# Kernel tuning notes

Hardware: AMD Instinct MI355X
Metric: run time of the kernel (lower is better)

Reference implementation:

```python
import jax, jax.numpy as jnp
import numpy as np

N_NODES = 50000
N_EDGES = 800000
IN_FEATS = 256
OUT_FEATS = 32
NUM_HEADS = 8
NUM_ETYPES = 5


def setup_inputs() -> dict:
    key = jax.random.key(0)
    k1, k2, k3, k4, k5, k6 = jax.random.split(key, 6)
    feat = jax.random.normal(k1, (N_NODES, IN_FEATS), dtype=jnp.float32)
    # xavier_normal-ish scale for fc weight [H*D, in]
    fc_w = jax.random.normal(k2, (NUM_HEADS * OUT_FEATS, IN_FEATS), dtype=jnp.float32) * 0.088
    edge_emb = jax.random.normal(k3, (NUM_ETYPES, NUM_HEADS), dtype=jnp.float32)
    e_feat = jax.random.randint(k4, (N_EDGES,), 0, NUM_ETYPES)
    src = jax.random.randint(k5, (N_EDGES,), 0, N_NODES)
    dst = jax.random.randint(k6, (N_EDGES,), 0, N_NODES)
    return {"feat": feat, "fc_w": fc_w, "edge_emb": edge_emb,
            "e_feat": e_feat, "src": src, "dst": dst}


def reference(feat, fc_w, edge_emb, e_feat, src, dst):
    N = feat.shape[0]
    H, D = NUM_HEADS, OUT_FEATS
    # fc: [N, in] @ [in, H*D] -> [N, H, D]
    feat_src = (feat @ fc_w.T).reshape(N, H, D)
    # per-edge, per-head logits from edge-type embedding: [E, H]
    e = edge_emb[e_feat]
    # edge_softmax: softmax over incoming edges of each dst node, per head
    m = jax.ops.segment_max(e, dst, num_segments=N)          # [N, H]
    ex = jnp.exp(e - m[dst])                                  # [E, H]
    denom = jax.ops.segment_sum(ex, dst, num_segments=N)     # [N, H]
    attn = ex / denom[dst]                                    # [E, H]
    # attn_sum: sum of attention weights arriving at each dst (== 1 w/o dropout)
    attn_sum = jax.ops.segment_sum(attn, dst, num_segments=N)  # [N, H]
    # weighted aggregation: sum_e attn_e * feat_src[src_e]
    msg = feat_src[src] * attn[:, :, None]                    # [E, H, D]
    agg = jax.ops.segment_sum(msg, dst, num_segments=N)      # [N, H, D]
    rst = agg / (attn_sum[:, :, None] + 1e-12)
    return rst, attn
```

## Files before the change

kernel.cpp:

```cpp
#include <hip/hip_runtime.h>

typedef unsigned short u16;
typedef unsigned int u32;
typedef __attribute__((ext_vector_type(8))) short bf16x8;
typedef __attribute__((ext_vector_type(4))) float f32x4;
typedef __attribute__((ext_vector_type(2))) float f32x2;

#define NND 50000
#define NE 800000
#define NH 8
#define ND 32
#define NTY 5
#define NV (NND * 4)
#define SQSH 14

__device__ inline u16 f2bf(float x){
  u32 u = __float_as_uint(x);
  return (u16)((u + 0x7FFFu + ((u >> 16) & 1u)) >> 16);
}

__global__ __launch_bounds__(256) void wcvt_k(const float* __restrict__ W,
                                              u16* __restrict__ Wb){
  int i = (blockIdx.x * 256 + threadIdx.x) * 4;
  f32x4 v = __builtin_nontemporal_load((const f32x4*)(W + i));
  ushort4 h = make_ushort4(f2bf(v[0]), f2bf(v[1]), f2bf(v[2]), f2bf(v[3]));
  *(ushort4*)(Wb + i) = h;
}

__global__ __launch_bounds__(512, 4) void gemm_k(const float* __restrict__ A,
                                                 const u16* __restrict__ Wb,
                                                 u16* __restrict__ C, int M){
  __shared__ u16 As[128 * 64];
  __shared__ u16 Ws[256 * 64];
  const int tid  = threadIdx.x;
  const int m0   = blockIdx.x * 128;
  const int lane = tid & 63, wid = tid >> 6;
  const int wm = (wid >> 2) * 64, wn = (wid & 3) * 64;
  const int ml = lane & 15, quad = lane >> 4;

  f32x4 acc[4][4] = {};

  const int ra = tid >> 2, ca0 = (tid & 3) * 2;
  int rag = m0 + ra; if (rag >= M) rag = M - 1;
  const float* aRow = A + (size_t)rag * 256;
  const int rw = tid >> 1, hw = tid & 1;
  const u16* wRow = Wb + (size_t)rw * 256;

  for (int k0 = 0; k0 < 256; k0 += 64){
    #pragma unroll
    for (int q = 0; q < 2; q++){
      int ch = ca0 + q;
      f32x4 v0 = __builtin_nontemporal_load((const f32x4*)(aRow + k0 + ch * 8));
      f32x4 v1 = __builtin_nontemporal_load((const f32x4*)(aRow + k0 + ch * 8 + 4));
      ushort4 h0 = make_ushort4(f2bf(v0[0]), f2bf(v0[1]), f2bf(v0[2]), f2bf(v0[3]));
      ushort4 h1 = make_ushort4(f2bf(v1[0]), f2bf(v1[1]), f2bf(v1[2]), f2bf(v1[3]));
      u16* p = As + ra * 64 + ((ch ^ (ra & 7)) * 8);
      *(ushort4*)p = h0;
      *(ushort4*)(p + 4) = h1;
    }
    #pragma unroll
    for (int q = 0; q < 4; q++){
      int ch = hw * 4 + q;
      uint4 wv = *(const uint4*)(wRow + k0 + ch * 8);
      *(uint4*)(Ws + rw * 64 + ((ch ^ (rw & 7)) * 8)) = wv;
    }
    __syncthreads();
    #pragma unroll
    for (int kk = 0; kk < 64; kk += 32){
      bf16x8 af[4], wf[4];
      const int cA = (kk >> 3) + quad;
      #pragma unroll
      for (int t = 0; t < 4; t++){
        int r = wm + t * 16 + ml;
        af[t] = *(const bf16x8*)(As + r * 64 + ((cA ^ (r & 7)) * 8));
      }
      #pragma unroll
      for (int t = 0; t < 4; t++){
        int n = wn + t * 16 + ml;
        wf[t] = *(const bf16x8*)(Ws + n * 64 + ((cA ^ (n & 7)) * 8));
      }
      #pragma unroll
      for (int i = 0; i < 4; i++)
        #pragma unroll
        for (int j = 0; j < 4; j++)
          acc[i][j] = __builtin_amdgcn_mfma_f32_16x16x32_bf16(af[i], wf[j], acc[i][j], 0, 0, 0);
    }
    __syncthreads();
  }
  const size_t qoff = (size_t)(wn >> 6) * NND * 64;
  #pragma unroll
  for (int i = 0; i < 4; i++){
    #pragma unroll
    for (int rr = 0; rr < 4; rr++){
      int row = m0 + wm + i * 16 + quad * 4 + rr;
      if (row < M){
        u16* crow = C + qoff + (size_t)row * 64;
        #pragma unroll
        for (int j = 0; j < 4; j++)
          __builtin_nontemporal_store(f2bf(acc[i][j][rr]), crow + j * 16 + ml);
      }
    }
  }
}

__global__ __launch_bounds__(256) void count_k(const int* __restrict__ dst,
                                               const int* __restrict__ src,
                                               int* __restrict__ deg4,
                                               int* __restrict__ epos){
  int e = blockIdx.x * 256 + threadIdx.x;
  if (e < NE){
    int v = dst[e] * 4 + (src[e] >> SQSH);
    epos[e] = atomicAdd(&deg4[v], 1);
  }
}

__global__ __launch_bounds__(256) void scan1_k(const int* __restrict__ deg4,
                                               int* __restrict__ offs4,
                                               int* __restrict__ bsum){
  __shared__ int lds[256];
  int b = blockIdx.x, tid = threadIdx.x;
  int base = b * 1024 + tid * 4;
  int d[4]; int tsum = 0;
  #pragma unroll
  for (int j = 0; j < 4; j++){
    int v = (base + j < NV) ? deg4[base + j] : 0;
    d[j] = tsum; tsum += v;
  }
  lds[tid] = tsum; __syncthreads();
  for (int off = 1; off < 256; off <<= 1){
    int v = (tid >= off) ? lds[tid - off] : 0;
    __syncthreads();
    lds[tid] += v;
    __syncthreads();
  }
  int excl = lds[tid] - tsum;
  #pragma unroll
  for (int j = 0; j < 4; j++)
    if (base + j < NV) offs4[base + j] = excl + d[j];
  if (tid == 255) bsum[b] = lds[tid];
}

__global__ __launch_bounds__(256) void scan2_k(const int* __restrict__ bsum,
                                               int* __restrict__ bbase, int nb){
  __shared__ int l[256];
  int tid = threadIdx.x;
  int v = (tid < nb) ? bsum[tid] : 0;
  l[tid] = v; __syncthreads();
  for (int off = 1; off < 256; off <<= 1){
    int u = (tid >= off) ? l[tid - off] : 0;
    __syncthreads();
    l[tid] += u;
    __syncthreads();
  }
  bbase[tid] = l[tid] - v;
}

__global__ __launch_bounds__(256) void scatter_k(const int* __restrict__ dst,
                                                 const int* __restrict__ src,
                                                 const int* __restrict__ ef,
                                                 const int* __restrict__ epos,
                                                 const int* __restrict__ offs4,
                                                 const int* __restrict__ bbase4,
                                                 int* __restrict__ csr){
  int e = blockIdx.x * 256 + threadIdx.x;
  if (e >= NE) return;
  int sv = src[e];
  int v = dst[e] * 4 + (sv >> SQSH);
  int pos = offs4[v] + bbase4[v >> 10] + epos[e];
  csr[pos] = (sv << 7) | ef[e];
}

__global__ __launch_bounds__(256) void attn_k(const int* __restrict__ dst,
                                              const int* __restrict__ ef,
                                              const float* __restrict__ rdq,
                                              const float* __restrict__ emb,
                                              float* __restrict__ attn){
  __shared__ float wl[40];
  int tid = threadIdx.x;
  if (tid < 40){
    int t = tid >> 3, h = tid & 7;
    float m = emb[h];
    for (int tt = 1; tt < NTY; ++tt) m = fmaxf(m, emb[tt * 8 + h]);
    wl[tid] = expf(emb[t * 8 + h] - m);
  }
  __syncthreads();
  int e = blockIdx.x * 256 + tid;
  if (e >= NE) return;
  int d = dst[e], t = ef[e];
  const float* wr = wl + t * 8;
  f32x4 o0, o1;
  #pragma unroll
  for (int q = 0; q < 4; q++){
    float2 rv = *(const float2*)(rdq + ((size_t)q * NND + d) * 2);
    float a = wr[2 * q] * rv.x, b = wr[2 * q + 1] * rv.y;
    if (q < 2){ o0[2 * q] = a; o0[2 * q + 1] = b; }
    else      { o1[2 * (q - 2)] = a; o1[2 * (q - 2) + 1] = b; }
  }
  __builtin_nontemporal_store(o0, (f32x4*)(attn + (size_t)e * 8));
  __builtin_nontemporal_store(o1, (f32x4*)(attn + (size_t)e * 8 + 4));
}

__device__ inline void acc8(uint4 v, float wt, f32x2* a){
  f32x2 w2; w2.x = wt; w2.y = wt;
  f32x2 t0; t0.x = __uint_as_float(v.x << 16); t0.y = __uint_as_float(v.x & 0xFFFF0000u);
  f32x2 t1; t1.x = __uint_as_float(v.y << 16); t1.y = __uint_as_float(v.y & 0xFFFF0000u);
  f32x2 t2; t2.x = __uint_as_float(v.z << 16); t2.y = __uint_as_float(v.z & 0xFFFF0000u);
  f32x2 t3; t3.x = __uint_as_float(v.w << 16); t3.y = __uint_as_float(v.w & 0xFFFF0000u);
  a[0] += w2 * t0; a[1] += w2 * t1; a[2] += w2 * t2; a[3] += w2 * t3;
}

#define NBLK ((NND + 31) / 32)
#define NBH  ((NBLK + 1) / 2)

__global__ __launch_bounds__(256) void agg_k(const u16* __restrict__ fsrc,
                                             const int* __restrict__ csr,
                                             const int* __restrict__ offs4,
                                             const int* __restrict__ bbase4,
                                             const int* __restrict__ deg4,
                                             const float* __restrict__ emb,
                                             float* __restrict__ rst,
                                             float* __restrict__ rdq){
  __shared__ float wl[40];
  int tid = threadIdx.x;
  if (tid < 40){
    int t = tid >> 3, h = tid & 7;
    float m = emb[h];
    for (int tt = 1; tt < NTY; ++tt) m = fmaxf(m, emb[tt * 8 + h]);
    wl[tid] = expf(emb[t * 8 + h] - m);
  }
  __syncthreads();
  const int c  = blockIdx.x & 7;
  const int q  = c >> 1;
  const int nb = (blockIdx.x >> 3) * 2 + (c & 1);
  int node = nb * 32 + (tid >> 3);
  if (node >= NND) return;
  const int sl = tid & 7;
  const int h  = 2 * q + (sl >> 2);
  const u16* qbase = fsrc + (size_t)q * (NND * 64) + sl * 8;
  const int v0 = node * 4;
  int s = offs4[v0] + bbase4[v0 >> 10];
  int4 dg = *(const int4*)(deg4 + v0);
  int e = s + dg.x + dg.y + dg.z + dg.w;
  f32x2 a[4]; a[0] = 0.f; a[1] = 0.f; a[2] = 0.f; a[3] = 0.f;
  float ss = 0.f;
  int i = s;
  for (; i + 3 < e; i += 4){
    int p0 = csr[i], p1 = csr[i+1], p2 = csr[i+2], p3 = csr[i+3];
    uint4 v0g = *(const uint4*)(qbase + ((size_t)(p0 >> 7) << 6));
    uint4 v1g = *(const uint4*)(qbase + ((size_t)(p1 >> 7) << 6));
    uint4 v2g = *(const uint4*)(qbase + ((size_t)(p2 >> 7) << 6));
    uint4 v3g = *(const uint4*)(qbase + ((size_t)(p3 >> 7) << 6));
    float w0 = wl[(p0 & 7) * 8 + h];
    float w1 = wl[(p1 & 7) * 8 + h];
    float w2 = wl[(p2 & 7) * 8 + h];
    float w3 = wl[(p3 & 7) * 8 + h];
    acc8(v0g, w0, a); acc8(v1g, w1, a); acc8(v2g, w2, a); acc8(v3g, w3, a);
    ss += (w0 + w1) + (w2 + w3);
  }
  for (; i < e; i++){
    int p0 = csr[i];
    uint4 v0g = *(const uint4*)(qbase + ((size_t)(p0 >> 7) << 6));
    float w0 = wl[(p0 & 7) * 8 + h];
    acc8(v0g, w0, a);
    ss += w0;
  }
  float inv = 1.0f / (ss + 1e-12f);
  f32x4 o0, o1;
  o0[0] = a[0].x*inv; o0[1] = a[0].y*inv; o0[2] = a[1].x*inv; o0[3] = a[1].y*inv;
  o1[0] = a[2].x*inv; o1[1] = a[2].y*inv; o1[2] = a[3].x*inv; o1[3] = a[3].y*inv;
  float* orow = rst + (size_t)node * 256 + q * 64 + sl * 8;
  __builtin_nontemporal_store(o0, (f32x4*)orow);
  __builtin_nontemporal_store(o1, (f32x4*)(orow + 4));
  if ((sl & 3) == 0)
    __builtin_nontemporal_store(inv, rdq + ((size_t)q * NND + node) * 2 + (sl >> 2));
}

extern "C" void kernel_launch(void* const* d_in, const int* in_sizes, int n_in,
                              void* d_out, int out_size, void* d_ws, size_t ws_size,
                              hipStream_t stream) {
  const float* feat = (const float*)d_in[0];
  const float* fcw  = (const float*)d_in[1];
  const float* emb  = (const float*)d_in[2];
  const int*   ef   = (const int*)d_in[3];
  const int*   src  = (const int*)d_in[4];
  const int*   dst  = (const int*)d_in[5];

  float* rst  = (float*)d_out;
  float* attn = (float*)d_out + (size_t)NND * NH * ND;

  char* ws = (char*)d_ws;
  size_t o = 0;
  u16* fsrc    = (u16*)(ws + o);   o += (size_t)NND * 256 * 2;
  int* csr     = (int*)(ws + o);   o += (size_t)NE * 4;
  int* epos    = (int*)(ws + o);   o += (size_t)NE * 4;
  int* offs4   = (int*)(ws + o);   o += (size_t)NV * 4 + 256;
  int* deg4    = (int*)(ws + o);   o += (size_t)NV * 4 + 256;
  float* rdq   = (float*)(ws + o); o += (size_t)NND * NH * 4;
  u16* wb      = (u16*)(ws + o);   o += (size_t)256 * 256 * 2;
  int* bsum    = (int*)(ws + o);   o += 1024;
  int* bbase4  = (int*)(ws + o);   o += 1024;

  hipMemsetAsync(deg4, 0, (size_t)NV * 4, stream);

  wcvt_k<<<64, 256, 0, stream>>>(fcw, wb);
  gemm_k<<<391, 512, 0, stream>>>(feat, wb, fsrc, NND);
  count_k<<<(NE + 255) / 256, 256, 0, stream>>>(dst, src, deg4, epos);
  scan1_k<<<(NV + 1023) / 1024, 256, 0, stream>>>(deg4, offs4, bsum);
  scan2_k<<<1, 256, 0, stream>>>(bsum, bbase4, (NV + 1023) / 1024);
  scatter_k<<<(NE + 255) / 256, 256, 0, stream>>>(dst, src, ef, epos, offs4, bbase4, csr);
  agg_k<<<8 * NBH, 256, 0, stream>>>(fsrc, csr, offs4, bbase4, deg4, emb, rst, rdq);
  attn_k<<<(NE + 255) / 256, 256, 0, stream>>>(dst, ef, rdq, emb, attn);
}
```

Measured before the change: 263.2 us.

## Sort nodes by degree for aggregation and use atomic cursors in scatter

Adds a prep kernel that bins nodes by in-degree within chunks of 1024 and writes a permutation, so agg_k groups nodes of similar degree into the same wavefront and warps diverge less. Scatter now claims CSR slots with atomic cursors instead of a per-edge position array saved from count_k, which removes the epos buffer and its read and write. agg_k takes its edge range from the post-scatter cursors. The cost is an extra kernel launch, more scattered node access in agg_k, and a CSR edge order within each segment that is no longer deterministic.

```diff
diff --git a/kernel.cpp b/kernel.cpp
--- a/kernel.cpp
+++ b/kernel.cpp
@@ -105,18 +105,16 @@
 
 __global__ __launch_bounds__(256) void count_k(const int* __restrict__ dst,
                                                const int* __restrict__ src,
-                                               int* __restrict__ deg4,
-                                               int* __restrict__ epos){
+                                               int* __restrict__ deg4){
   int e = blockIdx.x * 256 + threadIdx.x;
-  if (e < NE){
-    int v = dst[e] * 4 + (src[e] >> SQSH);
-    epos[e] = atomicAdd(&deg4[v], 1);
-  }
+  if (e < NE)
+    atomicAdd(&deg4[dst[e] * 4 + (src[e] >> SQSH)], 1);
 }
 
 __global__ __launch_bounds__(256) void scan1_k(const int* __restrict__ deg4,
                                                int* __restrict__ offs4,
-                                               int* __restrict__ bsum){
+                                               int* __restrict__ bsum,
+                                               int* __restrict__ degn){
   __shared__ int lds[256];
   int b = blockIdx.x, tid = threadIdx.x;
   int base = b * 1024 + tid * 4;
@@ -126,6 +124,8 @@
     int v = (base + j < NV) ? deg4[base + j] : 0;
     d[j] = tsum; tsum += v;
   }
+  int node = b * 256 + tid;
+  if (node < NND) degn[node] = tsum;
   lds[tid] = tsum; __syncthreads();
   for (int off = 1; off < 256; off <<= 1){
     int v = (tid >= off) ? lds[tid - off] : 0;
@@ -155,18 +155,60 @@
   bbase[tid] = l[tid] - v;
 }
 
+__global__ __launch_bounds__(256) void prep_k(const int* __restrict__ degn,
+                                              const int* __restrict__ offs4,
+                                              const int* __restrict__ bbase4,
+                                              int* __restrict__ cursor,
+                                              int* __restrict__ nperm){
+  __shared__ int hist[64], hcur[64];
+  int b = blockIdx.x, tid = threadIdx.x;
+  int vbase = b * 4096;
+  #pragma unroll
+  for (int j = 0; j < 16; j++){
+    int v = vbase + tid + j * 256;
+    if (v < NV) cursor[v] = offs4[v] + bbase4[v >> 10];
+  }
+  if (tid < 64) hist[tid] = 0;
+  __syncthreads();
+  int n0 = b * 1024;
+  int myn[4], mybin[4];
+  #pragma unroll
+  for (int j = 0; j < 4; j++){
+    int idx = tid * 4 + j;
+    int n = n0 + idx;
+    myn[j] = -1;
+    if (n < NND){
+      int dg = degn[n];
+      int bin = dg > 63 ? 63 : dg;
+      myn[j] = n; mybin[j] = bin;
+      atomicAdd(&hist[bin], 1);
+    }
+  }
+  __syncthreads();
+  if (tid == 0){
+    int acc = 0;
+    for (int i = 0; i < 64; i++){ int t = hist[i]; hcur[i] = acc; acc += t; }
+  }
+  __syncthreads();
+  #pragma unroll
+  for (int j = 0; j < 4; j++){
+    if (myn[j] >= 0){
+      int pos = n0 + atomicAdd(&hcur[mybin[j]], 1);
+      nperm[pos] = myn[j];
+    }
+  }
+}
+
 __global__ __launch_bounds__(256) void scatter_k(const int* __restrict__ dst,
                                                  const int* __restrict__ src,
                                                  const int* __restrict__ ef,
-                                                 const int* __restrict__ epos,
-                                                 const int* __restrict__ offs4,
-                                                 const int* __restrict__ bbase4,
+                                                 int* __restrict__ cursor,
                                                  int* __restrict__ csr){
   int e = blockIdx.x * 256 + threadIdx.x;
   if (e >= NE) return;
   int sv = src[e];
   int v = dst[e] * 4 + (sv >> SQSH);
-  int pos = offs4[v] + bbase4[v >> 10] + epos[e];
+  int pos = atomicAdd(&cursor[v], 1);
   csr[pos] = (sv << 7) | ef[e];
 }
 
@@ -214,9 +256,9 @@
 
 __global__ __launch_bounds__(256) void agg_k(const u16* __restrict__ fsrc,
                                              const int* __restrict__ csr,
-                                             const int* __restrict__ offs4,
-                                             const int* __restrict__ bbase4,
+                                             const int* __restrict__ cursor,
                                              const int* __restrict__ deg4,
+                                             const int* __restrict__ nperm,
                                              const float* __restrict__ emb,
                                              float* __restrict__ rst,
                                              float* __restrict__ rdq){
@@ -232,15 +274,17 @@
   const int c  = blockIdx.x & 7;
   const int q  = c >> 1;
   const int nb = (blockIdx.x >> 3) * 2 + (c & 1);
-  int node = nb * 32 + (tid >> 3);
-  if (node >= NND) return;
+  const int pidx = nb * 32 + (tid >> 3);
+  if (pidx >= NND) return;
+  const int node = nperm[pidx];
   const int sl = tid & 7;
   const int h  = 2 * q + (sl >> 2);
   const u16* qbase = fsrc + (size_t)q * (NND * 64) + sl * 8;
   const int v0 = node * 4;
-  int s = offs4[v0] + bbase4[v0 >> 10];
+  int4 c4 = *(const int4*)(cursor + v0);
   int4 dg = *(const int4*)(deg4 + v0);
-  int e = s + dg.x + dg.y + dg.z + dg.w;
+  int s = c4.x - dg.x;
+  int e = c4.w;
   f32x2 a[4]; a[0] = 0.f; a[1] = 0.f; a[2] = 0.f; a[3] = 0.f;
   float ss = 0.f;
   int i = s;
@@ -292,10 +336,12 @@
   size_t o = 0;
   u16* fsrc    = (u16*)(ws + o);   o += (size_t)NND * 256 * 2;
   int* csr     = (int*)(ws + o);   o += (size_t)NE * 4;
-  int* epos    = (int*)(ws + o);   o += (size_t)NE * 4;
   int* offs4   = (int*)(ws + o);   o += (size_t)NV * 4 + 256;
   int* deg4    = (int*)(ws + o);   o += (size_t)NV * 4 + 256;
+  int* cursor  = (int*)(ws + o);   o += (size_t)NV * 4 + 4096;
   float* rdq   = (float*)(ws + o); o += (size_t)NND * NH * 4;
+  int* degn    = (int*)(ws + o);   o += (size_t)NND * 4 + 1024;
+  int* nperm   = (int*)(ws + o);   o += (size_t)NND * 4 + 1024;
   u16* wb      = (u16*)(ws + o);   o += (size_t)256 * 256 * 2;
   int* bsum    = (int*)(ws + o);   o += 1024;
   int* bbase4  = (int*)(ws + o);   o += 1024;
@@ -304,10 +350,11 @@
 
   wcvt_k<<<64, 256, 0, stream>>>(fcw, wb);
   gemm_k<<<391, 512, 0, stream>>>(feat, wb, fsrc, NND);
-  count_k<<<(NE + 255) / 256, 256, 0, stream>>>(dst, src, deg4, epos);
-  scan1_k<<<(NV + 1023) / 1024, 256, 0, stream>>>(deg4, offs4, bsum);
+  count_k<<<(NE + 255) / 256, 256, 0, stream>>>(dst, src, deg4);
+  scan1_k<<<(NV + 1023) / 1024, 256, 0, stream>>>(deg4, offs4, bsum, degn);
   scan2_k<<<1, 256, 0, stream>>>(bsum, bbase4, (NV + 1023) / 1024);
-  scatter_k<<<(NE + 255) / 256, 256, 0, stream>>>(dst, src, ef, epos, offs4, bbase4, csr);
-  agg_k<<<8 * NBH, 256, 0, stream>>>(fsrc, csr, offs4, bbase4, deg4, emb, rst, rdq);
+  prep_k<<<(NND + 1023) / 1024, 256, 0, stream>>>(degn, offs4, bbase4, cursor, nperm);
+  scatter_k<<<(NE + 255) / 256, 256, 0, stream>>>(dst, src, ef, cursor, csr);
+  agg_k<<<8 * NBH, 256, 0, stream>>>(fsrc, csr, cursor, deg4, nperm, emb, rst, rdq);
   attn_k<<<(NE + 255) / 256, 256, 0, stream>>>(dst, ef, rdq, emb, attn);
 }
```

Result: slower. 299.4 us (+13.8%).

## Build CSR with atomic cursors and sort nodes by degree in aggregation

Applied to the files above, without the earlier changes.

The count kernel no longer records a per-edge position. A new prep kernel materialises absolute bucket cursors, and the scatter kernel claims slots with atomicAdd on those cursors, removing the epos array and its write and read traffic. The aggregation kernel reads segment bounds from the post-scatter cursors. Within each block it ranks the 32 nodes by degree so that similar-degree nodes share a wavefront, which should reduce divergence. The trade-off is an extra launch, a second round of scatter atomics, and non-deterministic edge order within buckets.

```diff
diff --git a/kernel.cpp b/kernel.cpp
--- a/kernel.cpp
+++ b/kernel.cpp
@@ -105,13 +105,10 @@
 
 __global__ __launch_bounds__(256) void count_k(const int* __restrict__ dst,
                                                const int* __restrict__ src,
-                                               int* __restrict__ deg4,
-                                               int* __restrict__ epos){
+                                               int* __restrict__ deg4){
   int e = blockIdx.x * 256 + threadIdx.x;
-  if (e < NE){
-    int v = dst[e] * 4 + (src[e] >> SQSH);
-    epos[e] = atomicAdd(&deg4[v], 1);
-  }
+  if (e < NE)
+    atomicAdd(&deg4[dst[e] * 4 + (src[e] >> SQSH)], 1);
 }
 
 __global__ __launch_bounds__(256) void scan1_k(const int* __restrict__ deg4,
@@ -155,18 +152,23 @@
   bbase[tid] = l[tid] - v;
 }
 
+__global__ __launch_bounds__(256) void prep_k(const int* __restrict__ offs4,
+                                              const int* __restrict__ bbase4,
+                                              int* __restrict__ cursor){
+  int v = blockIdx.x * 256 + threadIdx.x;
+  if (v < NV) cursor[v] = offs4[v] + bbase4[v >> 10];
+}
+
 __global__ __launch_bounds__(256) void scatter_k(const int* __restrict__ dst,
                                                  const int* __restrict__ src,
                                                  const int* __restrict__ ef,
-                                                 const int* __restrict__ epos,
-                                                 const int* __restrict__ offs4,
-                                                 const int* __restrict__ bbase4,
+                                                 int* __restrict__ cursor,
                                                  int* __restrict__ csr){
   int e = blockIdx.x * 256 + threadIdx.x;
   if (e >= NE) return;
   int sv = src[e];
   int v = dst[e] * 4 + (sv >> SQSH);
-  int pos = offs4[v] + bbase4[v >> 10] + epos[e];
+  int pos = atomicAdd(&cursor[v], 1);
   csr[pos] = (sv << 7) | ef[e];
 }
 
@@ -214,13 +216,15 @@
 
 __global__ __launch_bounds__(256) void agg_k(const u16* __restrict__ fsrc,
                                              const int* __restrict__ csr,
-                                             const int* __restrict__ offs4,
-                                             const int* __restrict__ bbase4,
+                                             const int* __restrict__ cursor,
                                              const int* __restrict__ deg4,
                                              const float* __restrict__ emb,
                                              float* __restrict__ rst,
                                              float* __restrict__ rdq){
   __shared__ float wl[40];
+  __shared__ int sdg[32];
+  __shared__ int sse[32][2];
+  __shared__ int sidx[32];
   int tid = threadIdx.x;
   if (tid < 40){
     int t = tid >> 3, h = tid & 7;
@@ -228,19 +232,43 @@
     for (int tt = 1; tt < NTY; ++tt) m = fmaxf(m, emb[tt * 8 + h]);
     wl[tid] = expf(emb[t * 8 + h] - m);
   }
-  __syncthreads();
   const int c  = blockIdx.x & 7;
   const int q  = c >> 1;
   const int nb = (blockIdx.x >> 3) * 2 + (c & 1);
-  int node = nb * 32 + (tid >> 3);
+  if (tid < 32){
+    int node = nb * 32 + tid;
+    int s = 0, e = 0;
+    if (node < NND){
+      int v0 = node * 4;
+      int4 c4 = *(const int4*)(cursor + v0);
+      int4 dg = *(const int4*)(deg4 + v0);
+      s = c4.x - dg.x;
+      e = c4.w;
+    }
+    sse[tid][0] = s; sse[tid][1] = e;
+    sdg[tid] = e - s;
+  }
+  __syncthreads();
+  if (tid < 32){
+    int mydg = sdg[tid];
+    int r = 0;
+    #pragma unroll
+    for (int j = 0; j < 32; j++){
+      int dj = sdg[j];
+      r += (dj > mydg) || (dj == mydg && j < tid);
+    }
+    sidx[r] = tid;
+  }
+  __syncthreads();
+  const int gi = tid >> 3;
+  const int li = sidx[gi];
+  const int node = nb * 32 + li;
   if (node >= NND) return;
   const int sl = tid & 7;
   const int h  = 2 * q + (sl >> 2);
   const u16* qbase = fsrc + (size_t)q * (NND * 64) + sl * 8;
-  const int v0 = node * 4;
-  int s = offs4[v0] + bbase4[v0 >> 10];
-  int4 dg = *(const int4*)(deg4 + v0);
-  int e = s + dg.x + dg.y + dg.z + dg.w;
+  int s = sse[li][0];
+  int e = sse[li][1];
   f32x2 a[4]; a[0] = 0.f; a[1] = 0.f; a[2] = 0.f; a[3] = 0.f;
   float ss = 0.f;
   int i = s;
@@ -292,9 +320,9 @@
   size_t o = 0;
   u16* fsrc    = (u16*)(ws + o);   o += (size_t)NND * 256 * 2;
   int* csr     = (int*)(ws + o);   o += (size_t)NE * 4;
-  int* epos    = (int*)(ws + o);   o += (size_t)NE * 4;
   int* offs4   = (int*)(ws + o);   o += (size_t)NV * 4 + 256;
   int* deg4    = (int*)(ws + o);   o += (size_t)NV * 4 + 256;
+  int* cursor  = (int*)(ws + o);   o += (size_t)NV * 4 + 256;
   float* rdq   = (float*)(ws + o); o += (size_t)NND * NH * 4;
   u16* wb      = (u16*)(ws + o);   o += (size_t)256 * 256 * 2;
   int* bsum    = (int*)(ws + o);   o += 1024;
@@ -304,10 +332,11 @@
 
   wcvt_k<<<64, 256, 0, stream>>>(fcw, wb);
   gemm_k<<<391, 512, 0, stream>>>(feat, wb, fsrc, NND);
-  count_k<<<(NE + 255) / 256, 256, 0, stream>>>(dst, src, deg4, epos);
+  count_k<<<(NE + 255) / 256, 256, 0, stream>>>(dst, src, deg4);
   scan1_k<<<(NV + 1023) / 1024, 256, 0, stream>>>(deg4, offs4, bsum);
   scan2_k<<<1, 256, 0, stream>>>(bsum, bbase4, (NV + 1023) / 1024);
-  scatter_k<<<(NE + 255) / 256, 256, 0, stream>>>(dst, src, ef, epos, offs4, bbase4, csr);
-  agg_k<<<8 * NBH, 256, 0, stream>>>(fsrc, csr, offs4, bbase4, deg4, emb, rst, rdq);
+  prep_k<<<(NV + 255) / 256, 256, 0, stream>>>(offs4, bbase4, cursor);
+  scatter_k<<<(NE + 255) / 256, 256, 0, stream>>>(dst, src, ef, cursor, csr);
+  agg_k<<<8 * NBH, 256, 0, stream>>>(fsrc, csr, cursor, deg4, emb, rst, rdq);
   attn_k<<<(NE + 255) / 256, 256, 0, stream>>>(dst, ef, rdq, emb, attn);
 }
```

Measured after the change: 286.6 us. 1.09x slower.

## Build CSR via two-level LDS bucket sort instead of global atomics

Applied to the files above, without the earlier changes.

Replaces the per-edge global atomic degree count, scan and scatter with a two-level counting sort. A per-chunk LDS histogram over 64-node bins feeds a scanned bin-by-chunk matrix, edges are scattered into bins with LDS atomics, and a per-bin pass then sorts them into node order and writes explicit node offsets. This removes the memset and the contended global atomics, and lets the aggregation read offsets directly. In exchange it adds an extra pass over the edges, launches fewer and larger scatter blocks, and drops the old source-quadrant sub-ordering that may have helped gather locality.

```diff
diff --git a/kernel.cpp b/kernel.cpp
--- a/kernel.cpp
+++ b/kernel.cpp
@@ -11,8 +11,10 @@
 #define NH 8
 #define ND 32
 #define NTY 5
-#define NV (NND * 4)
-#define SQSH 14
+#define NBIN 782
+#define CHK 4096
+#define NCH 196
+#define NM (NBIN * NCH)
 
 __device__ inline u16 f2bf(float x){
   u32 u = __float_as_uint(x);
@@ -103,19 +105,24 @@
   }
 }
 
-__global__ __launch_bounds__(256) void count_k(const int* __restrict__ dst,
-                                               const int* __restrict__ src,
-                                               int* __restrict__ deg4,
-                                               int* __restrict__ epos){
-  int e = blockIdx.x * 256 + threadIdx.x;
-  if (e < NE){
-    int v = dst[e] * 4 + (src[e] >> SQSH);
-    epos[e] = atomicAdd(&deg4[v], 1);
-  }
-}
-
-__global__ __launch_bounds__(256) void scan1_k(const int* __restrict__ deg4,
-                                               int* __restrict__ offs4,
+__global__ __launch_bounds__(256) void hist_k(const int* __restrict__ dst,
+                                              int* __restrict__ mat){
+  __shared__ int h[NBIN];
+  int b = blockIdx.x, tid = threadIdx.x;
+  for (int i = tid; i < NBIN; i += 256) h[i] = 0;
+  __syncthreads();
+  int base = b * CHK;
+  #pragma unroll
+  for (int j = 0; j < CHK / 256; j++){
+    int e = base + j * 256 + tid;
+    if (e < NE) atomicAdd(&h[dst[e] >> 6], 1);
+  }
+  __syncthreads();
+  for (int i = tid; i < NBIN; i += 256) mat[i * NCH + b] = h[i];
+}
+
+__global__ __launch_bounds__(256) void scan1_k(const int* __restrict__ in,
+                                               int* __restrict__ out,
                                                int* __restrict__ bsum){
   __shared__ int lds[256];
   int b = blockIdx.x, tid = threadIdx.x;
@@ -123,7 +130,7 @@
   int d[4]; int tsum = 0;
   #pragma unroll
   for (int j = 0; j < 4; j++){
-    int v = (base + j < NV) ? deg4[base + j] : 0;
+    int v = (base + j < NM) ? in[base + j] : 0;
     d[j] = tsum; tsum += v;
   }
   lds[tid] = tsum; __syncthreads();
@@ -136,7 +143,7 @@
   int excl = lds[tid] - tsum;
   #pragma unroll
   for (int j = 0; j < 4; j++)
-    if (base + j < NV) offs4[base + j] = excl + d[j];
+    if (base + j < NM) out[base + j] = excl + d[j];
   if (tid == 255) bsum[b] = lds[tid];
 }
 
@@ -155,19 +162,64 @@
   bbase[tid] = l[tid] - v;
 }
 
-__global__ __launch_bounds__(256) void scatter_k(const int* __restrict__ dst,
-                                                 const int* __restrict__ src,
-                                                 const int* __restrict__ ef,
-                                                 const int* __restrict__ epos,
-                                                 const int* __restrict__ offs4,
-                                                 const int* __restrict__ bbase4,
-                                                 int* __restrict__ csr){
-  int e = blockIdx.x * 256 + threadIdx.x;
-  if (e >= NE) return;
-  int sv = src[e];
-  int v = dst[e] * 4 + (sv >> SQSH);
-  int pos = offs4[v] + bbase4[v >> 10] + epos[e];
-  csr[pos] = (sv << 7) | ef[e];
+__global__ __launch_bounds__(256) void scat_k(const int* __restrict__ dst,
+                                              const int* __restrict__ src,
+                                              const int* __restrict__ ef,
+                                              const int* __restrict__ mscan,
+                                              const int* __restrict__ bbase,
+                                              int* __restrict__ ebuf){
+  __shared__ int cur[NBIN];
+  int b = blockIdx.x, tid = threadIdx.x;
+  for (int i = tid; i < NBIN; i += 256){
+    int m = i * NCH + b;
+    cur[i] = mscan[m] + bbase[m >> 10];
+  }
+  __syncthreads();
+  int base = b * CHK;
+  #pragma unroll
+  for (int j = 0; j < CHK / 256; j++){
+    int e = base + j * 256 + tid;
+    if (e < NE){
+      int d = dst[e];
+      int r = atomicAdd(&cur[d >> 6], 1);
+      ebuf[r] = ((d & 63) << 19) | (src[e] << 3) | ef[e];
+    }
+  }
+}
+
+__global__ __launch_bounds__(256) void sort_k(const int* __restrict__ ebuf,
+                                              const int* __restrict__ mscan,
+                                              const int* __restrict__ bbase,
+                                              int* __restrict__ csr,
+                                              int* __restrict__ nodeoffs){
+  __shared__ int h[64], hc[64];
+  int b = blockIdx.x, tid = threadIdx.x;
+  int m0 = b * NCH;
+  int s = mscan[m0] + bbase[m0 >> 10];
+  int e;
+  if (b == NBIN - 1) e = NE;
+  else { int m1 = (b + 1) * NCH; e = mscan[m1] + bbase[m1 >> 10]; }
+  if (tid < 64) h[tid] = 0;
+  __syncthreads();
+  for (int i = s + tid; i < e; i += 256)
+    atomicAdd(&h[(ebuf[i] >> 19) & 63], 1);
+  __syncthreads();
+  if (tid == 0){
+    int acc = 0;
+    for (int k = 0; k < 64; k++){ int t = h[k]; hc[k] = acc; acc += t; }
+  }
+  __syncthreads();
+  if (tid < 64){
+    int node = b * 64 + tid;
+    if (node < NND) nodeoffs[node] = s + hc[tid];
+  }
+  if (b == NBIN - 1 && tid == 0) nodeoffs[NND] = NE;
+  __syncthreads();
+  for (int i = s + tid; i < e; i += 256){
+    int p = ebuf[i];
+    int r = atomicAdd(&hc[(p >> 19) & 63], 1);
+    csr[s + r] = p;
+  }
 }
 
 __global__ __launch_bounds__(256) void attn_k(const int* __restrict__ dst,
@@ -192,9 +244,9 @@
   #pragma unroll
   for (int q = 0; q < 4; q++){
     float2 rv = *(const float2*)(rdq + ((size_t)q * NND + d) * 2);
-    float a = wr[2 * q] * rv.x, b = wr[2 * q + 1] * rv.y;
-    if (q < 2){ o0[2 * q] = a; o0[2 * q + 1] = b; }
-    else      { o1[2 * (q - 2)] = a; o1[2 * (q - 2) + 1] = b; }
+    float a = wr[2 * q] * rv.x, bb = wr[2 * q + 1] * rv.y;
+    if (q < 2){ o0[2 * q] = a; o0[2 * q + 1] = bb; }
+    else      { o1[2 * (q - 2)] = a; o1[2 * (q - 2) + 1] = bb; }
   }
   __builtin_nontemporal_store(o0, (f32x4*)(attn + (size_t)e * 8));
   __builtin_nontemporal_store(o1, (f32x4*)(attn + (size_t)e * 8 + 4));
@@ -214,9 +266,7 @@
 
 __global__ __launch_bounds__(256) void agg_k(const u16* __restrict__ fsrc,
                                              const int* __restrict__ csr,
-                                             const int* __restrict__ offs4,
-                                             const int* __restrict__ bbase4,
-                                             const int* __restrict__ deg4,
+                                             const int* __restrict__ nodeoffs,
                                              const float* __restrict__ emb,
                                              float* __restrict__ rst,
                                              float* __restrict__ rdq){
@@ -237,19 +287,17 @@
   const int sl = tid & 7;
   const int h  = 2 * q + (sl >> 2);
   const u16* qbase = fsrc + (size_t)q * (NND * 64) + sl * 8;
-  const int v0 = node * 4;
-  int s = offs4[v0] + bbase4[v0 >> 10];
-  int4 dg = *(const int4*)(deg4 + v0);
-  int e = s + dg.x + dg.y + dg.z + dg.w;
+  int s = nodeoffs[node];
+  int e = nodeoffs[node + 1];
   f32x2 a[4]; a[0] = 0.f; a[1] = 0.f; a[2] = 0.f; a[3] = 0.f;
   float ss = 0.f;
   int i = s;
   for (; i + 3 < e; i += 4){
     int p0 = csr[i], p1 = csr[i+1], p2 = csr[i+2], p3 = csr[i+3];
-    uint4 v0g = *(const uint4*)(qbase + ((size_t)(p0 >> 7) << 6));
-    uint4 v1g = *(const uint4*)(qbase + ((size_t)(p1 >> 7) << 6));
-    uint4 v2g = *(const uint4*)(qbase + ((size_t)(p2 >> 7) << 6));
-    uint4 v3g = *(const uint4*)(qbase + ((size_t)(p3 >> 7) << 6));
+    uint4 v0g = *(const uint4*)(qbase + ((size_t)((p0 >> 3) & 0xFFFF) << 6));
+    uint4 v1g = *(const uint4*)(qbase + ((size_t)((p1 >> 3) & 0xFFFF) << 6));
+    uint4 v2g = *(const uint4*)(qbase + ((size_t)((p2 >> 3) & 0xFFFF) << 6));
+    uint4 v3g = *(const uint4*)(qbase + ((size_t)((p3 >> 3) & 0xFFFF) << 6));
     float w0 = wl[(p0 & 7) * 8 + h];
     float w1 = wl[(p1 & 7) * 8 + h];
     float w2 = wl[(p2 & 7) * 8 + h];
@@ -259,7 +307,7 @@
   }
   for (; i < e; i++){
     int p0 = csr[i];
-    uint4 v0g = *(const uint4*)(qbase + ((size_t)(p0 >> 7) << 6));
+    uint4 v0g = *(const uint4*)(qbase + ((size_t)((p0 >> 3) & 0xFFFF) << 6));
     float w0 = wl[(p0 & 7) * 8 + h];
     acc8(v0g, w0, a);
     ss += w0;
@@ -291,23 +339,23 @@
   char* ws = (char*)d_ws;
   size_t o = 0;
   u16* fsrc    = (u16*)(ws + o);   o += (size_t)NND * 256 * 2;
+  int* ebuf    = (int*)(ws + o);   o += (size_t)NE * 4;
   int* csr     = (int*)(ws + o);   o += (size_t)NE * 4;
-  int* epos    = (int*)(ws + o);   o += (size_t)NE * 4;
-  int* offs4   = (int*)(ws + o);   o += (size_t)NV * 4 + 256;
-  int* deg4    = (int*)(ws + o);   o += (size_t)NV * 4 + 256;
+  int* mat     = (int*)(ws + o);   o += (size_t)NM * 4 + 512;
+  int* mscan   = (int*)(ws + o);   o += (size_t)NM * 4 + 512;
   float* rdq   = (float*)(ws + o); o += (size_t)NND * NH * 4;
+  int* nodeoffs= (int*)(ws + o);   o += (size_t)(NND + 1) * 4 + 252;
   u16* wb      = (u16*)(ws + o);   o += (size_t)256 * 256 * 2;
   int* bsum    = (int*)(ws + o);   o += 1024;
-  int* bbase4  = (int*)(ws + o);   o += 1024;
-
-  hipMemsetAsync(deg4, 0, (size_t)NV * 4, stream);
+  int* bbase   = (int*)(ws + o);   o += 1024;
 
   wcvt_k<<<64, 256, 0, stream>>>(fcw, wb);
   gemm_k<<<391, 512, 0, stream>>>(feat, wb, fsrc, NND);
-  count_k<<<(NE + 255) / 256, 256, 0, stream>>>(dst, src, deg4, epos);
-  scan1_k<<<(NV + 1023) / 1024, 256, 0, stream>>>(deg4, offs4, bsum);
-  scan2_k<<<1, 256, 0, stream>>>(bsum, bbase4, (NV + 1023) / 1024);
-  scatter_k<<<(NE + 255) / 256, 256, 0, stream>>>(dst, src, ef, epos, offs4, bbase4, csr);
-  agg_k<<<8 * NBH, 256, 0, stream>>>(fsrc, csr, offs4, bbase4, deg4, emb, rst, rdq);
+  hist_k<<<NCH, 256, 0, stream>>>(dst, mat);
+  scan1_k<<<(NM + 1023) / 1024, 256, 0, stream>>>(mat, mscan, bsum);
+  scan2_k<<<1, 256, 0, stream>>>(bsum, bbase, (NM + 1023) / 1024);
+  scat_k<<<NCH, 256, 0, stream>>>(dst, src, ef, mscan, bbase, ebuf);
+  sort_k<<<NBIN, 256, 0, stream>>>(ebuf, mscan, bbase, csr, nodeoffs);
+  agg_k<<<8 * NBH, 256, 0, stream>>>(fsrc, csr, nodeoffs, emb, rst, rdq);
   attn_k<<<(NE + 255) / 256, 256, 0, stream>>>(dst, ef, rdq, emb, attn);
 }
```

New measurement: 246.7 us. 1.07x faster.
